# Performance work log

Measured on AMD Instinct MI355X. Metric: run time of the kernel, lower is better.

## Reference

```python
import jax, jax.numpy as jnp
import numpy as np

TEMPERATURE = 2.5  # TopKRouter temperature from MoELayer.__init__
TOPK = 2


def setup_inputs() -> dict:
    key = jax.random.key(0)
    ks = jax.random.split(key, 4)
    B, T, D, F, E = 8, 8192, 512, 2048, 8
    x = jax.random.normal(ks[0], (B, T, D), jnp.float32)
    Wr = jax.random.normal(ks[1], (D, E), jnp.float32) * (D ** -0.5)
    W1 = jax.random.normal(ks[2], (E, D, F), jnp.float32) * (D ** -0.5)
    b1 = jnp.zeros((E, F), jnp.float32)
    W2 = jax.random.normal(ks[3], (E, F, D), jnp.float32) * (F ** -0.5)
    b2 = jnp.zeros((E, D), jnp.float32)
    return {"x": x, "Wr": Wr, "W1": W1, "b1": b1, "W2": W2, "b2": b2}


def reference(x, Wr, W1, b1, W2, b2):
    # x: (B, T, D); eval-mode MoE: no router noise, no capacity, no dropout.
    B, T, D = x.shape
    E = Wr.shape[1]
    N = B * T
    xf = x.reshape(N, D)

    # Router: softmax(logits / temperature), then top-k, renormalize kept probs.
    logits = xf @ Wr                                  # (N, E)
    probs = jax.nn.softmax(logits / TEMPERATURE, axis=-1)
    topk_vals, topk_idx = jax.lax.top_k(probs, TOPK)  # (N, K)
    topk_vals = topk_vals / jnp.sum(topk_vals, axis=-1, keepdims=True)

    # Scatter top-k weights into per-expert combine weights w: (N, E).
    w = jnp.zeros((N, E), xf.dtype)
    w = w.at[jnp.arange(N)[:, None], topk_idx].add(topk_vals)

    # Weighted combine of expert FFN outputs (fixed small loop over E experts).
    out = jnp.zeros_like(xf)
    for e in range(E):
        h = jax.nn.gelu(xf @ W1[e] + b1[e])           # (N, F)
        out = out + w[:, e:e + 1] * (h @ W2[e] + b2[e])
    return out.reshape(B, T, D)
```

## Files before the change

### kernel.cpp

```cpp
#include <hip/hip_runtime.h>
#include <cstdint>
#include <cstddef>

#define N_TOK 65536
#define DIM 512
#define FF 2048
#define NE 8
#define HCAP 24576
#define MAXT 1032

typedef __attribute__((ext_vector_type(8))) short short8;
typedef __attribute__((ext_vector_type(4))) float f32x4;

__device__ __forceinline__ unsigned f2bf(float f) {
  unsigned u = __builtin_bit_cast(unsigned, f);
  u = u + 0x7fffu + ((u >> 16) & 1u);
  return (u >> 16) & 0xffffu;
}

__device__ __forceinline__ void gload_lds16(const void* g, void* l) {
  __builtin_amdgcn_global_load_lds((const __attribute__((address_space(1))) void*)g,
                                   (__attribute__((address_space(3))) void*)l, 16, 0, 0);
}

__global__ __launch_bounds__(256) void k_transpose_cast(
    const float* __restrict__ in, unsigned short* __restrict__ outp, int rows, int cols)
{
  __shared__ float tile[32][33];
  const float* ine = in + (size_t)blockIdx.z * rows * cols;
  unsigned short* oute = outp + (size_t)blockIdx.z * rows * cols;
  int tx = threadIdx.x & 31, ty = threadIdx.x >> 5;
  int r0 = blockIdx.y * 32, c0 = blockIdx.x * 32;
#pragma unroll
  for (int i = 0; i < 4; ++i)
    tile[ty + i*8][tx] = ine[(size_t)(r0 + ty + i*8)*cols + c0 + tx];
  __syncthreads();
#pragma unroll
  for (int i = 0; i < 4; ++i) {
    int r = c0 + ty + i*8, c = r0 + tx;
    oute[(size_t)r*rows + c] = (unsigned short)f2bf(tile[tx][ty + i*8]);
  }
}

__global__ __launch_bounds__(256) void k_router(
    const float* __restrict__ x, const float* __restrict__ Wr,
    unsigned short* __restrict__ xb, int2* __restrict__ tinfo, int* __restrict__ cnt)
{
  __shared__ int lcnt[8];
  int tid = threadIdx.x, lane = tid & 63, wv = tid >> 6;
  if (tid < 8) lcnt[tid] = 0;
  float wr[8][8];
#pragma unroll
  for (int j = 0; j < 8; ++j) {
    const float4* p = (const float4*)(Wr + (size_t)(lane*8 + j)*NE);
    float4 a = p[0], b = p[1];
    wr[j][0]=a.x; wr[j][1]=a.y; wr[j][2]=a.z; wr[j][3]=a.w;
    wr[j][4]=b.x; wr[j][5]=b.y; wr[j][6]=b.z; wr[j][7]=b.w;
  }
  __syncthreads();
  int t0 = blockIdx.x*64 + wv*16;
  for (int it = 0; it < 16; ++it) {
    int t = t0 + it;
    const float4* xp = (const float4*)(x + (size_t)t*DIM + lane*8);
    float4 v0 = xp[0], v1 = xp[1];
    float xv[8] = {v0.x,v0.y,v0.z,v0.w,v1.x,v1.y,v1.z,v1.w};
    uint4 pk;
    pk.x = f2bf(xv[0]) | (f2bf(xv[1]) << 16);
    pk.y = f2bf(xv[2]) | (f2bf(xv[3]) << 16);
    pk.z = f2bf(xv[4]) | (f2bf(xv[5]) << 16);
    pk.w = f2bf(xv[6]) | (f2bf(xv[7]) << 16);
    *(uint4*)(xb + (size_t)t*DIM + lane*8) = pk;
    float lg[8];
#pragma unroll
    for (int e2 = 0; e2 < 8; ++e2) lg[e2] = 0.f;
#pragma unroll
    for (int j = 0; j < 8; ++j)
#pragma unroll
      for (int e2 = 0; e2 < 8; ++e2) lg[e2] += xv[j]*wr[j][e2];
#pragma unroll
    for (int off = 32; off >= 1; off >>= 1)
#pragma unroll
      for (int e2 = 0; e2 < 8; ++e2) lg[e2] += __shfl_xor(lg[e2], off, 64);
    int e0 = 0; float v0m = lg[0];
#pragma unroll
    for (int e2 = 1; e2 < 8; ++e2) if (lg[e2] > v0m) { v0m = lg[e2]; e0 = e2; }
    int e1 = -1; float v1m = -3.0e38f;
#pragma unroll
    for (int e2 = 0; e2 < 8; ++e2) if (e2 != e0 && lg[e2] > v1m) { v1m = lg[e2]; e1 = e2; }
    float w0 = 1.f / (1.f + __expf((v1m - v0m) * 0.4f));
    if (lane == 0) {
      atomicAdd(&lcnt[e0], 1);
      atomicAdd(&lcnt[e1], 1);
      tinfo[t] = make_int2(e0 | (e1 << 8), __float_as_int(w0));
    }
  }
  __syncthreads();
  if (tid < 8) atomicAdd(&cnt[tid*16], lcnt[tid]);
}

__global__ void k_offsets(int* cnt) {
  if (threadIdx.x == 0) {
    int base = 0, tb = 0;
    for (int e2 = 0; e2 < 8; ++e2) {
      int c = cnt[e2*16]; if (c > HCAP) c = HCAP;
      cnt[e2*16 + 1] = base;
      base += cnt[e2*16];
      cnt[e2*16 + 2] = 0;
      cnt[e2*16 + 3] = tb;
      tb += (c + 127) >> 7;
    }
    cnt[135] = tb;
  }
}

__global__ __launch_bounds__(128) void k_fill(
    const int2* __restrict__ tinfo, int* __restrict__ tokl,
    float* __restrict__ pwl, int* __restrict__ cnt)
{
  __shared__ int lc[8], lbase[8], gb[8];
  __shared__ unsigned char ce[128];
  __shared__ int csl[128];
  __shared__ float cw[128];
  int tid = threadIdx.x;
  if (tid < 8) { lc[tid] = 0; gb[tid] = cnt[tid*16 + 1]; }
  __syncthreads();
  if (tid < 64) {
    int t = blockIdx.x*64 + tid;
    int2 inf = tinfo[t];
    int e0 = inf.x & 0xff, e1 = (inf.x >> 8) & 0xff;
    float w0 = __int_as_float(inf.y);
    int i0 = tid*2, i1 = i0 + 1;
    ce[i0] = (unsigned char)e0; cw[i0] = w0;        csl[i0] = atomicAdd(&lc[e0], 1);
    ce[i1] = (unsigned char)e1; cw[i1] = 1.f - w0;  csl[i1] = atomicAdd(&lc[e1], 1);
  }
  __syncthreads();
  if (tid < 8) lbase[tid] = atomicAdd(&cnt[tid*16 + 2], lc[tid]);
  __syncthreads();
  int e = ce[tid];
  int p = gb[e] + lbase[e] + csl[tid];
  tokl[p] = blockIdx.x*64 + (tid >> 1);
  pwl[p]  = cw[tid];
}

__device__ __forceinline__ void stage128(
    const unsigned short* __restrict__ src, size_t stride, int k0,
    unsigned short* __restrict__ buf, int tid)
{
#pragma unroll
  for (int j = 0; j < 4; ++j) {
    int lrow = j*32 + (tid >> 3);
    gload_lds16(src + (size_t)lrow*stride + k0 + (((tid & 7) ^ (lrow & 7)) << 3),
                buf + j*2048 + tid*8);
  }
}

__device__ __forceinline__ int tile_expert(const int* cnt, int gt) {
  int e = 0;
#pragma unroll
  for (int k = 1; k < 8; ++k) if (gt >= cnt[k*16 + 3]) e = k;
  return e;
}

__global__ __launch_bounds__(256, 2) void k_gemm1(
    const unsigned short* __restrict__ xb, const unsigned short* __restrict__ w1t,
    const float* __restrict__ b1, const int* __restrict__ cnt,
    const int* __restrict__ tokl, unsigned short* __restrict__ h, int T0, int cap)
{
  const int bid = blockIdx.x;
  const int n  = (bid & 7) | (((bid >> 3) & 1) << 3);
  const int lt = bid >> 4;
  const int gt = T0 + lt;
  if (lt >= cap || gt >= cnt[135]) return;
  const int e = tile_expert(cnt, gt);
  const int m = gt - cnt[e*16 + 3];
  const int count0 = cnt[e*16];
  const int count = count0 < HCAP ? count0 : HCAP;
  const int row0 = m*128;
  const int gbase = cnt[e*16 + 1];

  __shared__ __align__(16) unsigned short lds[32768];
  unsigned short* As = lds;
  unsigned short* Bs = lds + 16384;

  const int tid = threadIdx.x, lane = tid & 63, wv = tid >> 6;
  const int r16 = lane & 15, g4 = lane >> 4;
  const int wm = wv >> 1, wn = wv & 1;

  int rows4[4];
#pragma unroll
  for (int j = 0; j < 4; ++j) {
    int rr = row0 + j*32 + (tid >> 3);
    if (rr > count - 1) rr = count - 1;
    rows4[j] = tokl[gbase + rr];
  }
  const int axor = ((tid & 7) ^ ((tid >> 3) & 7)) << 3;
  const unsigned short* w1p = w1t + (size_t)e*FF*DIM + (size_t)(n*128)*DIM;

  auto stageA = [&](unsigned short* buf, int k0) {
#pragma unroll
    for (int j = 0; j < 4; ++j)
      gload_lds16(xb + (size_t)rows4[j]*DIM + k0 + axor, buf + j*2048 + tid*8);
  };

  const f32x4 fz = {0.f, 0.f, 0.f, 0.f};
  f32x4 acc[4][4];
#pragma unroll
  for (int a = 0; a < 4; ++a)
#pragma unroll
    for (int b = 0; b < 4; ++b) acc[a][b] = fz;

  stageA(As, 0);
  stage128(w1p, DIM, 0, Bs, tid);
  __syncthreads();
  int buf = 0;
  for (int kk = 0; kk < DIM/64; ++kk) {
    if (kk + 1 < DIM/64) {
      stageA(As + (buf ^ 1)*8192, (kk + 1)*64);
      stage128(w1p, DIM, (kk + 1)*64, Bs + (buf ^ 1)*8192, tid);
    }
    const unsigned short* ab = As + buf*8192;
    const unsigned short* bb = Bs + buf*8192;
    short8 af[4][2], bf[4][2];
#pragma unroll
    for (int mf = 0; mf < 4; ++mf) {
      int row = wm*64 + mf*16 + r16;
#pragma unroll
      for (int k2 = 0; k2 < 2; ++k2)
        af[mf][k2] = *(const short8*)(ab + row*64 + ((((k2 << 2) + g4) ^ (row & 7)) << 3));
    }
#pragma unroll
    for (int nf = 0; nf < 4; ++nf) {
      int row = wn*64 + nf*16 + r16;
#pragma unroll
      for (int k2 = 0; k2 < 2; ++k2)
        bf[nf][k2] = *(const short8*)(bb + row*64 + ((((k2 << 2) + g4) ^ (row & 7)) << 3));
    }
    __builtin_amdgcn_s_setprio(1);
#pragma unroll
    for (int k2 = 0; k2 < 2; ++k2)
#pragma unroll
      for (int mf = 0; mf < 4; ++mf)
#pragma unroll
        for (int nf = 0; nf < 4; ++nf)
          acc[mf][nf] = __builtin_amdgcn_mfma_f32_16x16x32_bf16(
              af[mf][k2], bf[nf][k2], acc[mf][nf], 0, 0, 0);
    __builtin_amdgcn_s_setprio(0);
    __syncthreads();
    buf ^= 1;
  }

  float b1v[4];
#pragma unroll
  for (int nf = 0; nf < 4; ++nf)
    b1v[nf] = b1[(size_t)e*FF + n*128 + wn*64 + nf*16 + r16];

  unsigned short* hs = lds;
#pragma unroll
  for (int mf = 0; mf < 4; ++mf)
#pragma unroll
    for (int nf = 0; nf < 4; ++nf) {
      int col = wn*64 + nf*16 + r16;
#pragma unroll
      for (int i = 0; i < 4; ++i) {
        int row = wm*64 + mf*16 + g4*4 + i;
        float v = acc[mf][nf][i] + b1v[nf];
        float u = v * (0.7978845608028654f + 0.0356774081f*v*v);
        float gl = v * __builtin_amdgcn_rcpf(1.f + __expf(-2.f*u));
        hs[row*136 + col] = (unsigned short)f2bf(gl);
      }
    }
  __syncthreads();
  unsigned short* hdst = h + (size_t)lt*(128*FF);
#pragma unroll
  for (int j = 0; j < 8; ++j) {
    int o = j*256 + tid;
    int row = o >> 4, part = o & 15;
    if (row0 + row < count)
      *(uint4*)(hdst + (size_t)row*FF + n*128 + part*8) =
          *(const uint4*)(hs + row*136 + part*8);
  }
}

__global__ __launch_bounds__(256, 2) void k_gemm2(
    const unsigned short* __restrict__ h, const unsigned short* __restrict__ w2t,
    const float* __restrict__ b2, const int* __restrict__ tokl,
    const float* __restrict__ pwl, const int* __restrict__ cnt,
    float* __restrict__ out, int T0, int cap)
{
  const int bid = blockIdx.x;
  const int lt = (bid >> 5)*8 + (bid & 7);
  const int n  = (bid >> 3) & 3;
  const int gt = T0 + lt;
  if (lt >= cap || gt >= cnt[135]) return;
  const int e = tile_expert(cnt, gt);
  const int m = gt - cnt[e*16 + 3];
  const int count0 = cnt[e*16];
  const int count = count0 < HCAP ? count0 : HCAP;
  const int row0 = m*128;
  const int gbase = cnt[e*16 + 1];

  __shared__ __align__(16) unsigned short lds[32768];
  unsigned short* As = lds;
  unsigned short* Bs = lds + 16384;

  const int tid = threadIdx.x, lane = tid & 63, wv = tid >> 6;
  const int r16 = lane & 15, g4 = lane >> 4;
  const int wm = wv >> 1, wn = wv & 1;

  const unsigned short* ap = h + (size_t)lt*(128*FF);
  const unsigned short* bp = w2t + (size_t)e*DIM*FF + (size_t)(n*128)*FF;

  const f32x4 fz = {0.f, 0.f, 0.f, 0.f};
  f32x4 acc[4][4];
#pragma unroll
  for (int a = 0; a < 4; ++a)
#pragma unroll
    for (int b = 0; b < 4; ++b) acc[a][b] = fz;

  stage128(ap, FF, 0, As, tid);
  stage128(bp, FF, 0, Bs, tid);
  __syncthreads();
  int buf = 0;
  for (int kk = 0; kk < FF/64; ++kk) {
    if (kk + 1 < FF/64) {
      stage128(ap, FF, (kk + 1)*64, As + (buf ^ 1)*8192, tid);
      stage128(bp, FF, (kk + 1)*64, Bs + (buf ^ 1)*8192, tid);
    }
    const unsigned short* ab = As + buf*8192;
    const unsigned short* bb = Bs + buf*8192;
    short8 af[4][2], bf[4][2];
#pragma unroll
    for (int mf = 0; mf < 4; ++mf) {
      int row = wm*64 + mf*16 + r16;
#pragma unroll
      for (int k2 = 0; k2 < 2; ++k2)
        af[mf][k2] = *(const short8*)(ab + row*64 + ((((k2 << 2) + g4) ^ (row & 7)) << 3));
    }
#pragma unroll
    for (int nf = 0; nf < 4; ++nf) {
      int row = wn*64 + nf*16 + r16;
#pragma unroll
      for (int k2 = 0; k2 < 2; ++k2)
        bf[nf][k2] = *(const short8*)(bb + row*64 + ((((k2 << 2) + g4) ^ (row & 7)) << 3));
    }
    __builtin_amdgcn_s_setprio(1);
#pragma unroll
    for (int k2 = 0; k2 < 2; ++k2)
#pragma unroll
      for (int mf = 0; mf < 4; ++mf)
#pragma unroll
        for (int nf = 0; nf < 4; ++nf)
          acc[mf][nf] = __builtin_amdgcn_mfma_f32_16x16x32_bf16(
              af[mf][k2], bf[nf][k2], acc[mf][nf], 0, 0, 0);
    __builtin_amdgcn_s_setprio(0);
    __syncthreads();
    buf ^= 1;
  }

  float b2v[4];
#pragma unroll
  for (int nf = 0; nf < 4; ++nf)
    b2v[nf] = b2[(size_t)e*DIM + n*128 + wn*64 + nf*16 + r16];

#pragma unroll
  for (int mf = 0; mf < 4; ++mf)
#pragma unroll
    for (int i = 0; i < 4; ++i) {
      int lrow = row0 + wm*64 + mf*16 + g4*4 + i;
      if (lrow < count) {
        int tk = tokl[gbase + lrow];
        float wg = pwl[gbase + lrow];
#pragma unroll
        for (int nf = 0; nf < 4; ++nf) {
          int d = n*128 + wn*64 + nf*16 + r16;
          atomicAdd(out + (size_t)tk*DIM + d, (acc[mf][nf][i] + b2v[nf]) * wg);
        }
      }
    }
}

extern "C" void kernel_launch(void* const* d_in, const int* in_sizes, int n_in,
                              void* d_out, int out_size, void* d_ws, size_t ws_size,
                              hipStream_t stream)
{
  const float* x  = (const float*)d_in[0];
  const float* Wr = (const float*)d_in[1];
  const float* W1 = (const float*)d_in[2];
  const float* b1 = (const float*)d_in[3];
  const float* W2 = (const float*)d_in[4];
  const float* b2 = (const float*)d_in[5];
  float* out = (float*)d_out;
  (void)in_sizes; (void)n_in;

  char* ws = (char*)d_ws;
  unsigned short* xb  = (unsigned short*)(ws);
  unsigned short* w1t = (unsigned short*)(ws + 67108864);
  unsigned short* w2t = (unsigned short*)(ws + 83886080);
  int2*  tinfo = (int2*)(ws + 100663296);
  int*   tokl  = (int*)(ws + 101187584);
  float* pwl   = (float*)(ws + 101711872);
  int*   cnt   = (int*)(ws + 102236160);
  unsigned short* h = (unsigned short*)(ws + 102237184);

  const size_t FIXED = 102237184ULL;
  const size_t TILEB = (size_t)128 * FF * 2;
  long cap_l = (ws_size > FIXED) ? (long)((ws_size - FIXED) / TILEB) : 0;
  int cap = (int)(cap_l < MAXT ? cap_l : MAXT);
  if (cap > 256) cap = 256;
  if (cap < 8)  cap = 8;
  const int nch = (MAXT + cap - 1) / cap;
  const int ngrp = (cap + 7) / 8;

  hipMemsetAsync(cnt, 0, 256*sizeof(int), stream);
  hipMemsetAsync(d_out, 0, (size_t)out_size*sizeof(float), stream);

  dim3 g1(FF/32, DIM/32, NE);
  k_transpose_cast<<<g1, 256, 0, stream>>>(W1, w1t, DIM, FF);
  dim3 g2(DIM/32, FF/32, NE);
  k_transpose_cast<<<g2, 256, 0, stream>>>(W2, w2t, FF, DIM);

  k_router<<<N_TOK/64, 256, 0, stream>>>(x, Wr, xb, tinfo, cnt);
  k_offsets<<<1, 64, 0, stream>>>(cnt);
  k_fill<<<N_TOK/64, 128, 0, stream>>>(tinfo, tokl, pwl, cnt);

  for (int c = 0; c < nch; ++c) {
    const int T0 = c * cap;
    k_gemm1<<<ngrp*128, 256, 0, stream>>>(xb, w1t, b1, cnt, tokl, h, T0, cap);
    k_gemm2<<<ngrp*32,  256, 0, stream>>>(h, w2t, b2, tokl, pwl, cnt, out, T0, cap);
  }
}
```

Baseline: 1.145 ms.

## Fuse GEMM1 of next chunk with GEMM2 of previous chunk in one launch

Merges the two expert GEMM kernels into a single kernel whose blocks are split by index. Each launch runs the down-projection for chunk c-1 alongside the up-projection plus GELU for chunk c. The hidden buffer becomes a 256-slot ring indexed by global tile, with a fixed chunk size of 128 tiles, so the two stages use disjoint slots. The aim is to overlap the two stages, fill the GPU better and cut the tail idle time between dependent launches. In exchange, the workspace-size check is dropped and the code now assumes room for 256 hidden tiles.

New measurement: 1.146 ms. About the same (+0.1%).

```diff
diff --git a/kernel.cpp b/kernel.cpp
--- a/kernel.cpp
+++ b/kernel.cpp
@@ -8,6 +8,9 @@
 #define NE 8
 #define HCAP 24576
 #define MAXT 1032
+#define CAP 128
+#define NCH ((MAXT + CAP - 1) / CAP)
+#define HSLOTS 256
 
 typedef __attribute__((ext_vector_type(8))) short short8;
 typedef __attribute__((ext_vector_type(4))) float f32x4;
@@ -161,23 +164,45 @@
   return e;
 }
 
-__global__ __launch_bounds__(256, 2) void k_gemm1(
+__device__ __forceinline__ void mfma_step(
+    const unsigned short* __restrict__ ab, const unsigned short* __restrict__ bb,
+    f32x4 acc[4][4], int r16, int g4, int wm, int wn)
+{
+  short8 af[4][2], bf[4][2];
+#pragma unroll
+  for (int mf = 0; mf < 4; ++mf) {
+    int row = wm*64 + mf*16 + r16;
+#pragma unroll
+    for (int k2 = 0; k2 < 2; ++k2)
+      af[mf][k2] = *(const short8*)(ab + row*64 + ((((k2 << 2) + g4) ^ (row & 7)) << 3));
+  }
+#pragma unroll
+  for (int nf = 0; nf < 4; ++nf) {
+    int row = wn*64 + nf*16 + r16;
+#pragma unroll
+    for (int k2 = 0; k2 < 2; ++k2)
+      bf[nf][k2] = *(const short8*)(bb + row*64 + ((((k2 << 2) + g4) ^ (row & 7)) << 3));
+  }
+  __builtin_amdgcn_s_setprio(1);
+#pragma unroll
+  for (int k2 = 0; k2 < 2; ++k2)
+#pragma unroll
+    for (int mf = 0; mf < 4; ++mf)
+#pragma unroll
+      for (int nf = 0; nf < 4; ++nf)
+        acc[mf][nf] = __builtin_amdgcn_mfma_f32_16x16x32_bf16(
+            af[mf][k2], bf[nf][k2], acc[mf][nf], 0, 0, 0);
+  __builtin_amdgcn_s_setprio(0);
+}
+
+__global__ __launch_bounds__(256, 2) void k_step(
     const unsigned short* __restrict__ xb, const unsigned short* __restrict__ w1t,
-    const float* __restrict__ b1, const int* __restrict__ cnt,
-    const int* __restrict__ tokl, unsigned short* __restrict__ h, int T0, int cap)
-{
-  const int bid = blockIdx.x;
-  const int n  = (bid & 7) | (((bid >> 3) & 1) << 3);
-  const int lt = bid >> 4;
-  const int gt = T0 + lt;
-  if (lt >= cap || gt >= cnt[135]) return;
-  const int e = tile_expert(cnt, gt);
-  const int m = gt - cnt[e*16 + 3];
-  const int count0 = cnt[e*16];
-  const int count = count0 < HCAP ? count0 : HCAP;
-  const int row0 = m*128;
-  const int gbase = cnt[e*16 + 1];
-
+    const unsigned short* __restrict__ w2t, const float* __restrict__ b1,
+    const float* __restrict__ b2, const int* __restrict__ tokl,
+    const float* __restrict__ pwl, const int* __restrict__ cnt,
+    unsigned short* __restrict__ h, float* __restrict__ out,
+    int T0k2, int T0k1, int nb2)
+{
   __shared__ __align__(16) unsigned short lds[32768];
   unsigned short* As = lds;
   unsigned short* Bs = lds + 16384;
@@ -185,198 +210,143 @@
   const int tid = threadIdx.x, lane = tid & 63, wv = tid >> 6;
   const int r16 = lane & 15, g4 = lane >> 4;
   const int wm = wv >> 1, wn = wv & 1;
-
-  int rows4[4];
-#pragma unroll
-  for (int j = 0; j < 4; ++j) {
-    int rr = row0 + j*32 + (tid >> 3);
-    if (rr > count - 1) rr = count - 1;
-    rows4[j] = tokl[gbase + rr];
-  }
-  const int axor = ((tid & 7) ^ ((tid >> 3) & 7)) << 3;
-  const unsigned short* w1p = w1t + (size_t)e*FF*DIM + (size_t)(n*128)*DIM;
-
-  auto stageA = [&](unsigned short* buf, int k0) {
-#pragma unroll
-    for (int j = 0; j < 4; ++j)
-      gload_lds16(xb + (size_t)rows4[j]*DIM + k0 + axor, buf + j*2048 + tid*8);
-  };
-
   const f32x4 fz = {0.f, 0.f, 0.f, 0.f};
-  f32x4 acc[4][4];
-#pragma unroll
-  for (int a = 0; a < 4; ++a)
-#pragma unroll
-    for (int b = 0; b < 4; ++b) acc[a][b] = fz;
-
-  stageA(As, 0);
-  stage128(w1p, DIM, 0, Bs, tid);
-  __syncthreads();
-  int buf = 0;
-  for (int kk = 0; kk < DIM/64; ++kk) {
-    if (kk + 1 < DIM/64) {
-      stageA(As + (buf ^ 1)*8192, (kk + 1)*64);
-      stage128(w1p, DIM, (kk + 1)*64, Bs + (buf ^ 1)*8192, tid);
-    }
-    const unsigned short* ab = As + buf*8192;
-    const unsigned short* bb = Bs + buf*8192;
-    short8 af[4][2], bf[4][2];
-#pragma unroll
-    for (int mf = 0; mf < 4; ++mf) {
-      int row = wm*64 + mf*16 + r16;
-#pragma unroll
-      for (int k2 = 0; k2 < 2; ++k2)
-        af[mf][k2] = *(const short8*)(ab + row*64 + ((((k2 << 2) + g4) ^ (row & 7)) << 3));
-    }
-#pragma unroll
-    for (int nf = 0; nf < 4; ++nf) {
-      int row = wn*64 + nf*16 + r16;
-#pragma unroll
-      for (int k2 = 0; k2 < 2; ++k2)
-        bf[nf][k2] = *(const short8*)(bb + row*64 + ((((k2 << 2) + g4) ^ (row & 7)) << 3));
-    }
-    __builtin_amdgcn_s_setprio(1);
-#pragma unroll
-    for (int k2 = 0; k2 < 2; ++k2)
-#pragma unroll
-      for (int mf = 0; mf < 4; ++mf)
-#pragma unroll
-        for (int nf = 0; nf < 4; ++nf)
-          acc[mf][nf] = __builtin_amdgcn_mfma_f32_16x16x32_bf16(
-              af[mf][k2], bf[nf][k2], acc[mf][nf], 0, 0, 0);
-    __builtin_amdgcn_s_setprio(0);
+
+  if ((int)blockIdx.x < nb2) {
+    const int bid = blockIdx.x;
+    const int lt = (bid >> 5)*8 + (bid & 7);
+    const int n  = (bid >> 3) & 3;
+    const int gt = T0k2 + lt;
+    if (lt >= CAP || gt >= cnt[135]) return;
+    const int e = tile_expert(cnt, gt);
+    const int m = gt - cnt[e*16 + 3];
+    const int count0 = cnt[e*16];
+    const int count = count0 < HCAP ? count0 : HCAP;
+    const int row0 = m*128;
+    const int gbase = cnt[e*16 + 1];
+
+    const unsigned short* ap = h + (size_t)(gt & (HSLOTS - 1))*(128*FF);
+    const unsigned short* bp = w2t + (size_t)e*DIM*FF + (size_t)(n*128)*FF;
+
+    f32x4 acc[4][4];
+#pragma unroll
+    for (int a = 0; a < 4; ++a)
+#pragma unroll
+      for (int b = 0; b < 4; ++b) acc[a][b] = fz;
+
+    stage128(ap, FF, 0, As, tid);
+    stage128(bp, FF, 0, Bs, tid);
     __syncthreads();
-    buf ^= 1;
-  }
-
-  float b1v[4];
-#pragma unroll
-  for (int nf = 0; nf < 4; ++nf)
-    b1v[nf] = b1[(size_t)e*FF + n*128 + wn*64 + nf*16 + r16];
-
-  unsigned short* hs = lds;
-#pragma unroll
-  for (int mf = 0; mf < 4; ++mf)
-#pragma unroll
-    for (int nf = 0; nf < 4; ++nf) {
-      int col = wn*64 + nf*16 + r16;
+    int buf = 0;
+    for (int kk = 0; kk < FF/64; ++kk) {
+      if (kk + 1 < FF/64) {
+        stage128(ap, FF, (kk + 1)*64, As + (buf ^ 1)*8192, tid);
+        stage128(bp, FF, (kk + 1)*64, Bs + (buf ^ 1)*8192, tid);
+      }
+      mfma_step(As + buf*8192, Bs + buf*8192, acc, r16, g4, wm, wn);
+      __syncthreads();
+      buf ^= 1;
+    }
+
+    float b2v[4];
+#pragma unroll
+    for (int nf = 0; nf < 4; ++nf)
+      b2v[nf] = b2[(size_t)e*DIM + n*128 + wn*64 + nf*16 + r16];
+
+#pragma unroll
+    for (int mf = 0; mf < 4; ++mf)
 #pragma unroll
       for (int i = 0; i < 4; ++i) {
-        int row = wm*64 + mf*16 + g4*4 + i;
-        float v = acc[mf][nf][i] + b1v[nf];
-        float u = v * (0.7978845608028654f + 0.0356774081f*v*v);
-        float gl = v * __builtin_amdgcn_rcpf(1.f + __expf(-2.f*u));
-        hs[row*136 + col] = (unsigned short)f2bf(gl);
-      }
-    }
-  __syncthreads();
-  unsigned short* hdst = h + (size_t)lt*(128*FF);
-#pragma unroll
-  for (int j = 0; j < 8; ++j) {
-    int o = j*256 + tid;
-    int row = o >> 4, part = o & 15;
-    if (row0 + row < count)
-      *(uint4*)(hdst + (size_t)row*FF + n*128 + part*8) =
-          *(const uint4*)(hs + row*136 + part*8);
-  }
-}
-
-__global__ __launch_bounds__(256, 2) void k_gemm2(
-    const unsigned short* __restrict__ h, const unsigned short* __restrict__ w2t,
-    const float* __restrict__ b2, const int* __restrict__ tokl,
-    const float* __restrict__ pwl, const int* __restrict__ cnt,
-    float* __restrict__ out, int T0, int cap)
-{
-  const int bid = blockIdx.x;
-  const int lt = (bid >> 5)*8 + (bid & 7);
-  const int n  = (bid >> 3) & 3;
-  const int gt = T0 + lt;
-  if (lt >= cap || gt >= cnt[135]) return;
-  const int e = tile_expert(cnt, gt);
-  const int m = gt - cnt[e*16 + 3];
-  const int count0 = cnt[e*16];
-  const int count = count0 < HCAP ? count0 : HCAP;
-  const int row0 = m*128;
-  const int gbase = cnt[e*16 + 1];
-
-  __shared__ __align__(16) unsigned short lds[32768];
-  unsigned short* As = lds;
-  unsigned short* Bs = lds + 16384;
-
-  const int tid = threadIdx.x, lane = tid & 63, wv = tid >> 6;
-  const int r16 = lane & 15, g4 = lane >> 4;
-  const int wm = wv >> 1, wn = wv & 1;
-
-  const unsigned short* ap = h + (size_t)lt*(128*FF);
-  const unsigned short* bp = w2t + (size_t)e*DIM*FF + (size_t)(n*128)*FF;
-
-  const f32x4 fz = {0.f, 0.f, 0.f, 0.f};
-  f32x4 acc[4][4];
-#pragma unroll
-  for (int a = 0; a < 4; ++a)
-#pragma unroll
-    for (int b = 0; b < 4; ++b) acc[a][b] = fz;
-
-  stage128(ap, FF, 0, As, tid);
-  stage128(bp, FF, 0, Bs, tid);
-  __syncthreads();
-  int buf = 0;
-  for (int kk = 0; kk < FF/64; ++kk) {
-    if (kk + 1 < FF/64) {
-      stage128(ap, FF, (kk + 1)*64, As + (buf ^ 1)*8192, tid);
-      stage128(bp, FF, (kk + 1)*64, Bs + (buf ^ 1)*8192, tid);
-    }
-    const unsigned short* ab = As + buf*8192;
-    const unsigned short* bb = Bs + buf*8192;
-    short8 af[4][2], bf[4][2];
-#pragma unroll
-    for (int mf = 0; mf < 4; ++mf) {
-      int row = wm*64 + mf*16 + r16;
-#pragma unroll
-      for (int k2 = 0; k2 < 2; ++k2)
-        af[mf][k2] = *(const short8*)(ab + row*64 + ((((k2 << 2) + g4) ^ (row & 7)) << 3));
-    }
-#pragma unroll
-    for (int nf = 0; nf < 4; ++nf) {
-      int row = wn*64 + nf*16 + r16;
-#pragma unroll
-      for (int k2 = 0; k2 < 2; ++k2)
-        bf[nf][k2] = *(const short8*)(bb + row*64 + ((((k2 << 2) + g4) ^ (row & 7)) << 3));
-    }
-    __builtin_amdgcn_s_setprio(1);
-#pragma unroll
-    for (int k2 = 0; k2 < 2; ++k2)
-#pragma unroll
-      for (int mf = 0; mf < 4; ++mf)
-#pragma unroll
-        for (int nf = 0; nf < 4; ++nf)
-          acc[mf][nf] = __builtin_amdgcn_mfma_f32_16x16x32_bf16(
-              af[mf][k2], bf[nf][k2], acc[mf][nf], 0, 0, 0);
-    __builtin_amdgcn_s_setprio(0);
-    __syncthreads();
-    buf ^= 1;
-  }
-
-  float b2v[4];
-#pragma unroll
-  for (int nf = 0; nf < 4; ++nf)
-    b2v[nf] = b2[(size_t)e*DIM + n*128 + wn*64 + nf*16 + r16];
-
-#pragma unroll
-  for (int mf = 0; mf < 4; ++mf)
-#pragma unroll
-    for (int i = 0; i < 4; ++i) {
-      int lrow = row0 + wm*64 + mf*16 + g4*4 + i;
-      if (lrow < count) {
-        int tk = tokl[gbase + lrow];
-        float wg = pwl[gbase + lrow];
-#pragma unroll
-        for (int nf = 0; nf < 4; ++nf) {
-          int d = n*128 + wn*64 + nf*16 + r16;
-          atomicAdd(out + (size_t)tk*DIM + d, (acc[mf][nf][i] + b2v[nf]) * wg);
+        int lrow = row0 + wm*64 + mf*16 + g4*4 + i;
+        if (lrow < count) {
+          int tk = tokl[gbase + lrow];
+          float wg = pwl[gbase + lrow];
+#pragma unroll
+          for (int nf = 0; nf < 4; ++nf) {
+            int d = n*128 + wn*64 + nf*16 + r16;
+            atomicAdd(out + (size_t)tk*DIM + d, (acc[mf][nf][i] + b2v[nf]) * wg);
+          }
         }
       }
-    }
+  } else {
+    const int bid = blockIdx.x - nb2;
+    const int n  = (bid & 7) | (((bid >> 3) & 1) << 3);
+    const int lt = bid >> 4;
+    const int gt = T0k1 + lt;
+    if (lt >= CAP || gt >= cnt[135]) return;
+    const int e = tile_expert(cnt, gt);
+    const int m = gt - cnt[e*16 + 3];
+    const int count0 = cnt[e*16];
+    const int count = count0 < HCAP ? count0 : HCAP;
+    const int row0 = m*128;
+    const int gbase = cnt[e*16 + 1];
+
+    int rows4[4];
+#pragma unroll
+    for (int j = 0; j < 4; ++j) {
+      int rr = row0 + j*32 + (tid >> 3);
+      if (rr > count - 1) rr = count - 1;
+      rows4[j] = tokl[gbase + rr];
+    }
+    const int axor = ((tid & 7) ^ ((tid >> 3) & 7)) << 3;
+    const unsigned short* w1p = w1t + (size_t)e*FF*DIM + (size_t)(n*128)*DIM;
+
+    f32x4 acc[4][4];
+#pragma unroll
+    for (int a = 0; a < 4; ++a)
+#pragma unroll
+      for (int b = 0; b < 4; ++b) acc[a][b] = fz;
+
+#pragma unroll
+    for (int j = 0; j < 4; ++j)
+      gload_lds16(xb + (size_t)rows4[j]*DIM + axor, As + j*2048 + tid*8);
+    stage128(w1p, DIM, 0, Bs, tid);
+    __syncthreads();
+    int buf = 0;
+    for (int kk = 0; kk < DIM/64; ++kk) {
+      if (kk + 1 < DIM/64) {
+#pragma unroll
+        for (int j = 0; j < 4; ++j)
+          gload_lds16(xb + (size_t)rows4[j]*DIM + (kk + 1)*64 + axor,
+                      As + (buf ^ 1)*8192 + j*2048 + tid*8);
+        stage128(w1p, DIM, (kk + 1)*64, Bs + (buf ^ 1)*8192, tid);
+      }
+      mfma_step(As + buf*8192, Bs + buf*8192, acc, r16, g4, wm, wn);
+      __syncthreads();
+      buf ^= 1;
+    }
+
+    float b1v[4];
+#pragma unroll
+    for (int nf = 0; nf < 4; ++nf)
+      b1v[nf] = b1[(size_t)e*FF + n*128 + wn*64 + nf*16 + r16];
+
+    unsigned short* hs = lds;
+#pragma unroll
+    for (int mf = 0; mf < 4; ++mf)
+#pragma unroll
+      for (int nf = 0; nf < 4; ++nf) {
+        int col = wn*64 + nf*16 + r16;
+#pragma unroll
+        for (int i = 0; i < 4; ++i) {
+          int row = wm*64 + mf*16 + g4*4 + i;
+          float v = acc[mf][nf][i] + b1v[nf];
+          float u = v * (0.7978845608028654f + 0.0356774081f*v*v);
+          float gl = v * __builtin_amdgcn_rcpf(1.f + __expf(-2.f*u));
+          hs[row*136 + col] = (unsigned short)f2bf(gl);
+        }
+      }
+    __syncthreads();
+    unsigned short* hdst = h + (size_t)(gt & (HSLOTS - 1))*(128*FF);
+#pragma unroll
+    for (int j = 0; j < 8; ++j) {
+      int o = j*256 + tid;
+      int row = o >> 4, part = o & 15;
+      if (row0 + row < count)
+        *(uint4*)(hdst + (size_t)row*FF + n*128 + part*8) =
+            *(const uint4*)(hs + row*136 + part*8);
+    }
+  }
 }
 
 extern "C" void kernel_launch(void* const* d_in, const int* in_sizes, int n_in,
@@ -390,7 +360,7 @@
   const float* W2 = (const float*)d_in[4];
   const float* b2 = (const float*)d_in[5];
   float* out = (float*)d_out;
-  (void)in_sizes; (void)n_in;
+  (void)in_sizes; (void)n_in; (void)ws_size;
 
   char* ws = (char*)d_ws;
   unsigned short* xb  = (unsigned short*)(ws);
@@ -402,15 +372,6 @@
   int*   cnt   = (int*)(ws + 102236160);
   unsigned short* h = (unsigned short*)(ws + 102237184);
 
-  const size_t FIXED = 102237184ULL;
-  const size_t TILEB = (size_t)128 * FF * 2;
-  long cap_l = (ws_size > FIXED) ? (long)((ws_size - FIXED) / TILEB) : 0;
-  int cap = (int)(cap_l < MAXT ? cap_l : MAXT);
-  if (cap > 256) cap = 256;
-  if (cap < 8)  cap = 8;
-  const int nch = (MAXT + cap - 1) / cap;
-  const int ngrp = (cap + 7) / 8;
-
   hipMemsetAsync(cnt, 0, 256*sizeof(int), stream);
   hipMemsetAsync(d_out, 0, (size_t)out_size*sizeof(float), stream);
 
@@ -423,9 +384,10 @@
   k_offsets<<<1, 64, 0, stream>>>(cnt);
   k_fill<<<N_TOK/64, 128, 0, stream>>>(tinfo, tokl, pwl, cnt);
 
-  for (int c = 0; c < nch; ++c) {
-    const int T0 = c * cap;
-    k_gemm1<<<ngrp*128, 256, 0, stream>>>(xb, w1t, b1, cnt, tokl, h, T0, cap);
-    k_gemm2<<<ngrp*32,  256, 0, stream>>>(h, w2t, b2, tokl, pwl, cnt, out, T0, cap);
-  }
-}
+  for (int c = 0; c <= NCH; ++c) {
+    const int nb2 = (c > 0) ? CAP*4 : 0;
+    const int nb1 = (c < NCH) ? CAP*16 : 0;
+    k_step<<<nb2 + nb1, 256, 0, stream>>>(xb, w1t, w2t, b1, b2, tokl, pwl, cnt,
+                                          h, out, (c - 1)*CAP, c*CAP, nb2);
+  }
+}
```
